# Kernel optimization log

Measured on AMD Instinct MI355X. Metric: run time of the kernel, lower is better.

Reference implementation:

```python
import jax, jax.numpy as jnp
import numpy as np

DEPTH = 2
NW = 4          # number of wires (qubits), fixed by 2x2 patches
NP = 14 * 14    # patches per image
NUM_CLASSES = 10


def _ry(theta):
    c = jnp.cos(theta / 2).astype(jnp.complex64)
    s = jnp.sin(theta / 2).astype(jnp.complex64)
    return jnp.stack([jnp.stack([c, -s], -1), jnp.stack([s, c], -1)], -2)


def _rx(theta):
    c = jnp.cos(theta / 2).astype(jnp.complex64)
    s = (-1j) * jnp.sin(theta / 2).astype(jnp.complex64)
    return jnp.stack([jnp.stack([c, s], -1), jnp.stack([s, c], -1)], -2)


def _rz(theta):
    em = jnp.exp(-0.5j * theta.astype(jnp.complex64))
    ep = jnp.exp(0.5j * theta.astype(jnp.complex64))
    z = jnp.zeros_like(em)
    return jnp.stack([jnp.stack([em, z], -1), jnp.stack([z, ep], -1)], -2)


def _apply1(state, mat, wire):
    # state: (N,2,2,2,2); mat: (2,2) shared or (N,2,2) per-patch
    s = jnp.moveaxis(state, 1 + wire, -1)
    if mat.ndim == 2:
        s = jnp.einsum('...i,ji->...j', s, mat)
    else:
        s = jnp.einsum('n...i,nji->n...j', s, mat)
    return jnp.moveaxis(s, -1, 1 + wire)


def _cnot(state, c, t):
    a0 = jnp.take(state, 0, axis=1 + c)
    a1 = jnp.take(state, 1, axis=1 + c)
    t_ax = 1 + t - (1 if t > c else 0)   # target axis index after control removed
    a1 = jnp.flip(a1, axis=t_ax)
    return jnp.stack([a0, a1], axis=1 + c)


def _circuit(angles, params):
    # angles: (N,4) RY-encoded patch pixels; params: (DEPTH,NW,3)
    N = angles.shape[0]
    state = jnp.zeros((N, 16), jnp.complex64).at[:, 0].set(1.0).reshape(N, 2, 2, 2, 2)
    for w in range(NW):
        state = _apply1(state, _ry(angles[:, w]), w)
    for d in range(DEPTH):
        for w in range(NW):
            state = _apply1(state, _rx(params[d, w, 0]), w)
            state = _apply1(state, _ry(params[d, w, 1]), w)
            state = _apply1(state, _rz(params[d, w, 2]), w)
        for w in range(NW - 1):
            state = _cnot(state, w, w + 1)
        state = _cnot(state, NW - 1, 0)
    probs = state.real ** 2 + state.imag ** 2   # (N,2,2,2,2)
    feats = []
    for w in range(NW):
        p = jnp.moveaxis(probs, 1 + w, 1).reshape(N, 2, 8)
        feats.append(p[:, 0].sum(-1) - p[:, 1].sum(-1))  # <Z_w>
    return jnp.stack(feats, -1)                  # (N,4)


def setup_inputs() -> dict:
    key = jax.random.key(0)
    k1, k2, k3 = jax.random.split(key, 3)
    B = 4096
    x = jax.random.uniform(k1, (B, 1, 28, 28), jnp.float32)
    params = jax.random.normal(k2, (DEPTH, NW, 3), jnp.float32)
    W = jax.random.normal(k3, (NUM_CLASSES, NW * NP), jnp.float32) * 0.02
    b = jnp.zeros((NUM_CLASSES,), jnp.float32)
    return {"x": x, "params": params, "W": W, "b": b}


def reference(x, params, W, b):
    B = x.shape[0]
    # extract all 196 2x2 patches, row-major within each patch (matches view(bsz,-1))
    patches = x[:, 0].reshape(B, 14, 2, 14, 2).transpose(0, 1, 3, 2, 4).reshape(B * NP, 4)
    feats = _circuit(patches, params).reshape(B, NP * NW)  # (B,784)
    logits = feats @ W.T + b
    return jax.nn.log_softmax(logits, axis=-1)
```

## Files before the change

### kernel.cpp

```cpp
#include <hip/hip_runtime.h>
#include <hip/hip_bf16.h>

#define NPATCH 196

typedef float f2 __attribute__((ext_vector_type(2)));

__global__ __launch_bounds__(256) void quanv_setup(const float* __restrict__ P,
                                                   float* __restrict__ C) {
  __shared__ float gc[24], gs[24];
  __shared__ float Ur[8][2][2], Ui[8][2][2];
  __shared__ float Sr[2][16][16], Si[2][16][16];
  __shared__ float A[4][16][16];
  __shared__ float B0[4][3][8][8];
  __shared__ float B1[4][3][3][4][4];
  __shared__ float B2[4][3][3][3][2][2];
  const int tid = threadIdx.x;
  const int row = tid >> 4, col = tid & 15;

  if (tid < 24) {
    float s, c;
    __sincosf(0.5f * P[tid], &s, &c);
    gc[tid] = c; gs[tid] = s;
  }
  Sr[0][row][col] = (row == col) ? 1.0f : 0.0f;
  Si[0][row][col] = 0.0f;
  __syncthreads();

  if (tid < 8) {
    const int base = tid * 3;
    const float c1 = gc[base], s1 = gs[base];
    const float c2 = gc[base + 1], s2 = gs[base + 1];
    const float c3 = gc[base + 2], s3 = gs[base + 2];
    const float m00r = c2 * c1, m00i = s2 * s1;
    const float m01r = -s2 * c1, m01i = -c2 * s1;
    const float m10r = s2 * c1, m10i = -c2 * s1;
    const float m11r = c2 * c1, m11i = -s2 * s1;
    Ur[tid][0][0] = c3 * m00r + s3 * m00i;  Ui[tid][0][0] = c3 * m00i - s3 * m00r;
    Ur[tid][0][1] = c3 * m01r + s3 * m01i;  Ui[tid][0][1] = c3 * m01i - s3 * m01r;
    Ur[tid][1][0] = c3 * m10r - s3 * m10i;  Ui[tid][1][0] = c3 * m10i + s3 * m10r;
    Ur[tid][1][1] = c3 * m11r - s3 * m11i;  Ui[tid][1][1] = c3 * m11i + s3 * m11r;
  }
  __syncthreads();

  int cur = 0;
  for (int d = 0; d < 2; ++d) {
    for (int w = 0; w < 4; ++w) {
      const int gi = d * 4 + w;
      const int m = 8 >> w;
      const int bit = (row & m) ? 1 : 0;
      const int par = row ^ m;
      const int r0 = bit ? par : row, r1 = bit ? row : par;
      const float a_r = Sr[cur][r0][col], a_i = Si[cur][r0][col];
      const float b_r = Sr[cur][r1][col], b_i = Si[cur][r1][col];
      const float u0r = Ur[gi][bit][0], u0i = Ui[gi][bit][0];
      const float u1r = Ur[gi][bit][1], u1i = Ui[gi][bit][1];
      const float rn = u0r * a_r - u0i * a_i + u1r * b_r - u1i * b_i;
      const float in_ = u0r * a_i + u0i * a_r + u1r * b_i + u1i * b_r;
      Sr[cur ^ 1][row][col] = rn;
      Si[cur ^ 1][row][col] = in_;
      cur ^= 1;
      __syncthreads();
    }
    if (d == 0) {
      int k = row;
      k ^= (k & 1) ? 8 : 0;
      k ^= (k & 2) ? 1 : 0;
      k ^= (k & 4) ? 2 : 0;
      k ^= (k & 8) ? 4 : 0;
      const float pr_ = Sr[cur][k][col], pi_ = Si[cur][k][col];
      Sr[cur ^ 1][row][col] = pr_;
      Si[cur ^ 1][row][col] = pi_;
      cur ^= 1;
      __syncthreads();
    }
  }

  {
    const int i = row, j = col;
    float s0 = 0, s1 = 0, s2 = 0, s3 = 0;
#pragma unroll
    for (int k = 0; k < 16; ++k) {
      int gk = k;
      gk ^= (gk & 1) ? 8 : 0;
      gk ^= (gk & 2) ? 1 : 0;
      gk ^= (gk & 4) ? 2 : 0;
      gk ^= (gk & 8) ? 4 : 0;
      const float pr = Sr[cur][gk][i] * Sr[cur][gk][j] + Si[cur][gk][i] * Si[cur][gk][j];
      s0 += (k & 8) ? -pr : pr;
      s1 += (k & 4) ? -pr : pr;
      s2 += (k & 2) ? -pr : pr;
      s3 += (k & 1) ? -pr : pr;
    }
    A[0][i][j] = s0; A[1][i][j] = s1; A[2][i][j] = s2; A[3][i][j] = s3;
  }
  __syncthreads();

  {
    const int w = tid >> 6, ip = (tid >> 3) & 7, jp = tid & 7;
    const float a00 = A[w][ip][jp],     a11 = A[w][ip + 8][jp + 8];
    const float a01 = A[w][ip][jp + 8], a10 = A[w][ip + 8][jp];
    B0[w][0][ip][jp] = 0.5f * (a00 + a11);
    B0[w][1][ip][jp] = 0.5f * (a00 - a11);
    B0[w][2][ip][jp] = 0.5f * (a01 + a10);
  }
  __syncthreads();
  if (tid < 192) {
    const int w = tid / 48, a0 = (tid / 16) % 3, ii = (tid >> 2) & 3, jj = tid & 3;
    const float a00 = B0[w][a0][ii][jj],     a11 = B0[w][a0][ii + 4][jj + 4];
    const float a01 = B0[w][a0][ii][jj + 4], a10 = B0[w][a0][ii + 4][jj];
    B1[w][a0][0][ii][jj] = 0.5f * (a00 + a11);
    B1[w][a0][1][ii][jj] = 0.5f * (a00 - a11);
    B1[w][a0][2][ii][jj] = 0.5f * (a01 + a10);
  }
  __syncthreads();
  if (tid < 144) {
    const int w = tid / 36, a0 = (tid / 12) % 3, a1 = (tid / 4) % 3;
    const int i3 = (tid >> 1) & 1, j3 = tid & 1;
    const float a00 = B1[w][a0][a1][i3][j3],     a11 = B1[w][a0][a1][i3 + 2][j3 + 2];
    const float a01 = B1[w][a0][a1][i3][j3 + 2], a10 = B1[w][a0][a1][i3 + 2][j3];
    B2[w][a0][a1][0][i3][j3] = 0.5f * (a00 + a11);
    B2[w][a0][a1][1][i3][j3] = 0.5f * (a00 - a11);
    B2[w][a0][a1][2][i3][j3] = 0.5f * (a01 + a10);
  }
  __syncthreads();
  if (tid < 108) {
    const int w = tid / 27, r = tid % 27;
    const int a0 = r / 9, a1 = (r / 3) % 3, a2 = r % 3;
    const float a00 = B2[w][a0][a1][a2][0][0], a11 = B2[w][a0][a1][a2][1][1];
    const float a01 = B2[w][a0][a1][a2][0][1], a10 = B2[w][a0][a1][a2][1][0];
    const int base = (3 * a0 + a1) * 9 + 3 * a2;
    C[(base + 0) * 4 + w] = 0.5f * (a00 + a11);
    C[(base + 1) * 4 + w] = 0.5f * (a00 - a11);
    C[(base + 2) * 4 + w] = 0.5f * (a01 + a10);
  }
}

__global__ __launch_bounds__(256) void quanv_main(const float* __restrict__ x,
                                                  const float* __restrict__ W,
                                                  const float* __restrict__ bias,
                                                  const float* __restrict__ C,
                                                  float* __restrict__ out) {
  __shared__ float red2[49][10];
  __shared__ float logits[10];
  __shared__ float snorm;
  const int tid = threadIdx.x;
  const int b = blockIdx.x;

  float lg[10];
#pragma unroll
  for (int k = 0; k < 10; ++k) lg[k] = 0.0f;

  if (tid < NPATCH) {
    const int pi = tid / 14, pj = tid - pi * 14;
    const float* px = x + b * 784 + pi * 56 + pj * 2;
    const float2 r0 = *reinterpret_cast<const float2*>(px);
    const float2 r1 = *reinterpret_cast<const float2*>(px + 28);
    float c0, s0, c1, s1, c2, s2, c3, s3;
    __sincosf(r0.x, &s0, &c0);
    __sincosf(r0.y, &s1, &c1);
    __sincosf(r1.x, &s2, &c2);
    __sincosf(r1.y, &s3, &c3);
    const float m01s[9] = {1.0f, c1, s1, c0, c0 * c1, c0 * s1, s0, s0 * c1, s0 * s1};
    const float m23s[9] = {1.0f, c3, s3, c2, c2 * c3, c2 * s3, s2, s2 * c3, s2 * s3};
    f2 m23b[9];
#pragma unroll
    for (int q = 0; q < 9; ++q) m23b[q] = (f2){m23s[q], m23s[q]};

    f2 f01 = {0.0f, 0.0f}, f23 = {0.0f, 0.0f};
    const f2* C2 = reinterpret_cast<const f2*>(C);
#pragma unroll
    for (int a = 0; a < 9; ++a) {
      f2 t01 = {0.0f, 0.0f}, t23 = {0.0f, 0.0f};
#pragma unroll
      for (int q = 0; q < 9; ++q) {
        const int idx = (a * 9 + q) * 2;
        t01 += C2[idx] * m23b[q];
        t23 += C2[idx + 1] * m23b[q];
      }
      f01 += t01 * m01s[a];
      f23 += t23 * m01s[a];
    }
    const float f0 = f01.x, f1 = f01.y, f2v = f23.x, f3 = f23.y;

    const float* Wp = W + tid * 4;
#pragma unroll
    for (int k = 0; k < 10; ++k) {
      const float4 wv = *reinterpret_cast<const float4*>(Wp + k * 784);
      lg[k] = f0 * wv.x + f1 * wv.y + f2v * wv.z + f3 * wv.w;
    }
  }

#pragma unroll
  for (int k = 0; k < 10; ++k) {
    lg[k] += __shfl_xor(lg[k], 1);
    lg[k] += __shfl_xor(lg[k], 2);
  }
  if (tid < NPATCH) {
    const int g = tid >> 2, sub = tid & 3;
#pragma unroll
    for (int k = 0; k < 10; ++k)
      if ((k & 3) == sub) red2[g][k] = lg[k];
  }
  __syncthreads();
  if (tid < 10) {
    float s = bias[tid];
    for (int g2 = 0; g2 < 49; ++g2) s += red2[g2][tid];
    logits[tid] = s;
  }
  __syncthreads();
  if (tid == 0) {
    float m = logits[0];
#pragma unroll
    for (int k = 1; k < 10; ++k) m = fmaxf(m, logits[k]);
    float se = 0;
#pragma unroll
    for (int k = 0; k < 10; ++k) se += expf(logits[k] - m);
    snorm = m + logf(se);
  }
  __syncthreads();
  if (tid < 10) out[b * 10 + tid] = logits[tid] - snorm;
}

extern "C" void kernel_launch(void* const* d_in, const int* in_sizes, int n_in,
                              void* d_out, int out_size, void* d_ws, size_t ws_size,
                              hipStream_t stream) {
  const float* x = (const float*)d_in[0];
  const float* P = (const float*)d_in[1];
  const float* W = (const float*)d_in[2];
  const float* bias = (const float*)d_in[3];
  float* out = (float*)d_out;
  float* C = (float*)d_ws;
  const int B = out_size / 10;

  quanv_setup<<<1, 256, 0, stream>>>(P, C);
  quanv_main<<<B, 256, 0, stream>>>(x, W, bias, C, out);
}
```

Measured before the change: 24.43 us.

## Process eight images per block, keep W in registers, prefetch next image

Each block now handles eight images in turn. W rows and bias are loaded into registers once per block and reused, and the next image's pixels are prefetched while the current one is computed. The cross-patch reduction becomes two stages (70 threads, then 10 threads), with each of the 10 threads doing the softmax itself. This cuts repeated W loads and block launch overhead, but leaves only 512 blocks on the GPU and adds per-image barriers that serialize work inside a block.

```diff
diff --git a/kernel.cpp b/kernel.cpp
--- a/kernel.cpp
+++ b/kernel.cpp
@@ -2,8 +2,7 @@
 #include <hip/hip_bf16.h>
 
 #define NPATCH 196
-
-typedef float f2 __attribute__((ext_vector_type(2)));
+#define IMGS 8
 
 __global__ __launch_bounds__(256) void quanv_setup(const float* __restrict__ P,
                                                    float* __restrict__ C) {
@@ -135,90 +134,120 @@
   }
 }
 
-__global__ __launch_bounds__(256) void quanv_main(const float* __restrict__ x,
-                                                  const float* __restrict__ W,
-                                                  const float* __restrict__ bias,
-                                                  const float* __restrict__ C,
-                                                  float* __restrict__ out) {
+__global__ __launch_bounds__(256, 4) void quanv_main(const float* __restrict__ x,
+                                                     const float* __restrict__ W,
+                                                     const float* __restrict__ bias,
+                                                     const float* __restrict__ C,
+                                                     float* __restrict__ out,
+                                                     int B) {
   __shared__ float red2[49][10];
-  __shared__ float logits[10];
-  __shared__ float snorm;
+  __shared__ float red3[10][7];
   const int tid = threadIdx.x;
-  const int b = blockIdx.x;
-
-  float lg[10];
-#pragma unroll
-  for (int k = 0; k < 10; ++k) lg[k] = 0.0f;
-
-  if (tid < NPATCH) {
-    const int pi = tid / 14, pj = tid - pi * 14;
-    const float* px = x + b * 784 + pi * 56 + pj * 2;
-    const float2 r0 = *reinterpret_cast<const float2*>(px);
-    const float2 r1 = *reinterpret_cast<const float2*>(px + 28);
-    float c0, s0, c1, s1, c2, s2, c3, s3;
-    __sincosf(r0.x, &s0, &c0);
-    __sincosf(r0.y, &s1, &c1);
-    __sincosf(r1.x, &s2, &c2);
-    __sincosf(r1.y, &s3, &c3);
-    const float m01s[9] = {1.0f, c1, s1, c0, c0 * c1, c0 * s1, s0, s0 * c1, s0 * s1};
-    const float m23s[9] = {1.0f, c3, s3, c2, c2 * c3, c2 * s3, s2, s2 * c3, s2 * s3};
-    f2 m23b[9];
-#pragma unroll
-    for (int q = 0; q < 9; ++q) m23b[q] = (f2){m23s[q], m23s[q]};
-
-    f2 f01 = {0.0f, 0.0f}, f23 = {0.0f, 0.0f};
-    const f2* C2 = reinterpret_cast<const f2*>(C);
-#pragma unroll
-    for (int a = 0; a < 9; ++a) {
-      f2 t01 = {0.0f, 0.0f}, t23 = {0.0f, 0.0f};
-#pragma unroll
-      for (int q = 0; q < 9; ++q) {
-        const int idx = (a * 9 + q) * 2;
-        t01 += C2[idx] * m23b[q];
-        t23 += C2[idx + 1] * m23b[q];
+  const int b0 = blockIdx.x * IMGS;
+  const int active = (tid < NPATCH);
+
+  const int pi = tid / 14, pj = tid - pi * 14;
+  const int off = pi * 56 + pj * 2;
+
+  float4 wv[10];
+  if (active) {
+    const float* Wp = W + tid * 4;
+#pragma unroll
+    for (int k = 0; k < 10; ++k)
+      wv[k] = *reinterpret_cast<const float4*>(Wp + k * 784);
+  }
+  float biasr[10];
+#pragma unroll
+  for (int k = 0; k < 10; ++k) biasr[k] = bias[k];
+
+  const float4* C4 = reinterpret_cast<const float4*>(C);
+
+  float2 xa = {0.f, 0.f}, xb = {0.f, 0.f};
+  if (active && b0 < B) {
+    const float* px = x + b0 * 784 + off;
+    xa = *reinterpret_cast<const float2*>(px);
+    xb = *reinterpret_cast<const float2*>(px + 28);
+  }
+
+  for (int img = 0; img < IMGS; ++img) {
+    const int b = b0 + img;
+    if (b >= B) break;
+    const float2 ra = xa, rb = xb;
+    if (img + 1 < IMGS && active && b + 1 < B) {
+      const float* px = x + (b + 1) * 784 + off;
+      xa = *reinterpret_cast<const float2*>(px);
+      xb = *reinterpret_cast<const float2*>(px + 28);
+    }
+
+    float lg[10];
+#pragma unroll
+    for (int k = 0; k < 10; ++k) lg[k] = 0.0f;
+
+    if (active) {
+      float c0, s0, c1, s1, c2, s2, c3, s3;
+      __sincosf(ra.x, &s0, &c0);
+      __sincosf(ra.y, &s1, &c1);
+      __sincosf(rb.x, &s2, &c2);
+      __sincosf(rb.y, &s3, &c3);
+      const float m01[9] = {1.0f, c1, s1, c0, c0 * c1, c0 * s1, s0, s0 * c1, s0 * s1};
+      const float m23[9] = {1.0f, c3, s3, c2, c2 * c3, c2 * s3, s2, s2 * c3, s2 * s3};
+
+      float f0 = 0, f1 = 0, f2 = 0, f3 = 0;
+#pragma unroll
+      for (int a = 0; a < 9; ++a) {
+#pragma unroll
+        for (int q = 0; q < 9; ++q) {
+          const float pr = m01[a] * m23[q];
+          const float4 cc = C4[a * 9 + q];
+          f0 += cc.x * pr; f1 += cc.y * pr; f2 += cc.z * pr; f3 += cc.w * pr;
+        }
       }
-      f01 += t01 * m01s[a];
-      f23 += t23 * m01s[a];
-    }
-    const float f0 = f01.x, f1 = f01.y, f2v = f23.x, f3 = f23.y;
-
-    const float* Wp = W + tid * 4;
+#pragma unroll
+      for (int k = 0; k < 10; ++k)
+        lg[k] = f0 * wv[k].x + f1 * wv[k].y + f2 * wv[k].z + f3 * wv[k].w;
+    }
+
 #pragma unroll
     for (int k = 0; k < 10; ++k) {
-      const float4 wv = *reinterpret_cast<const float4*>(Wp + k * 784);
-      lg[k] = f0 * wv.x + f1 * wv.y + f2v * wv.z + f3 * wv.w;
-    }
-  }
-
-#pragma unroll
-  for (int k = 0; k < 10; ++k) {
-    lg[k] += __shfl_xor(lg[k], 1);
-    lg[k] += __shfl_xor(lg[k], 2);
-  }
-  if (tid < NPATCH) {
-    const int g = tid >> 2, sub = tid & 3;
-#pragma unroll
-    for (int k = 0; k < 10; ++k)
-      if ((k & 3) == sub) red2[g][k] = lg[k];
-  }
-  __syncthreads();
-  if (tid < 10) {
-    float s = bias[tid];
-    for (int g2 = 0; g2 < 49; ++g2) s += red2[g2][tid];
-    logits[tid] = s;
-  }
-  __syncthreads();
-  if (tid == 0) {
-    float m = logits[0];
-#pragma unroll
-    for (int k = 1; k < 10; ++k) m = fmaxf(m, logits[k]);
-    float se = 0;
-#pragma unroll
-    for (int k = 0; k < 10; ++k) se += expf(logits[k] - m);
-    snorm = m + logf(se);
-  }
-  __syncthreads();
-  if (tid < 10) out[b * 10 + tid] = logits[tid] - snorm;
+      lg[k] += __shfl_xor(lg[k], 1);
+      lg[k] += __shfl_xor(lg[k], 2);
+    }
+    if (active) {
+      const int g = tid >> 2, sub = tid & 3;
+#pragma unroll
+      for (int k = 0; k < 10; ++k)
+        if ((k & 3) == sub) red2[g][k] = lg[k];
+    }
+    __syncthreads();
+
+    if (tid < 70) {
+      const int k = tid / 7, part = tid - k * 7;
+      float s = 0.0f;
+#pragma unroll
+      for (int j = 0; j < 7; ++j) s += red2[part * 7 + j][k];
+      red3[k][part] = s;
+    }
+    __syncthreads();
+
+    if (tid < 10) {
+      float lgt[10];
+      float m = -1e30f;
+#pragma unroll
+      for (int kk = 0; kk < 10; ++kk) {
+        float s = biasr[kk];
+#pragma unroll
+        for (int j = 0; j < 7; ++j) s += red3[kk][j];
+        lgt[kk] = s;
+        m = fmaxf(m, s);
+      }
+      float se = 0.0f;
+#pragma unroll
+      for (int kk = 0; kk < 10; ++kk) se += expf(lgt[kk] - m);
+      const float sn = m + logf(se);
+      out[b * 10 + tid] = lgt[tid] - sn;
+    }
+    __syncthreads();
+  }
 }
 
 extern "C" void kernel_launch(void* const* d_in, const int* in_sizes, int n_in,
@@ -233,5 +262,5 @@
   const int B = out_size / 10;
 
   quanv_setup<<<1, 256, 0, stream>>>(P, C);
-  quanv_main<<<B, 256, 0, stream>>>(x, W, bias, C, out);
+  quanv_main<<<(B + IMGS - 1) / IMGS, 256, 0, stream>>>(x, W, bias, C, out, B);
 }
```

After: 44.32 us. 1.81x slower.
